# Performance work log

Hardware: AMD Instinct MI355X
Metric: run time of the kernel (lower is better)

The kernel has to match this reference:

```python
import jax, jax.numpy as jnp
import numpy as np

EMBED_DIM = 1024
NUM_HEADS = 16
HEAD_DIM = EMBED_DIM // NUM_HEADS


def setup_inputs() -> dict:
    key = jax.random.key(0)
    k_x, k_wqkv, k_bqkv, k_wo, k_bo = jax.random.split(key, 5)
    B, T, C = 4, 2048, EMBED_DIM
    s_in = 1.0 / np.sqrt(C)
    return {
        "x": jax.random.normal(k_x, (B, T, C), dtype=jnp.float32),
        # torch Linear: weight [out,in]; we store transposed [in,out] for x @ W
        "w_qkv": jax.random.uniform(k_wqkv, (C, 3 * C), dtype=jnp.float32, minval=-s_in, maxval=s_in),
        "b_qkv": jax.random.uniform(k_bqkv, (3 * C,), dtype=jnp.float32, minval=-s_in, maxval=s_in),
        "w_out": jax.random.uniform(k_wo, (C, C), dtype=jnp.float32, minval=-s_in, maxval=s_in),
        "b_out": jax.random.uniform(k_bo, (C,), dtype=jnp.float32, minval=-s_in, maxval=s_in),
    }


def reference(x, w_qkv, b_qkv, w_out, b_out):
    B, T, C = x.shape
    H, D = NUM_HEADS, HEAD_DIM
    qkv = x @ w_qkv + b_qkv                       # [B,T,3C]
    qkv = qkv.reshape(B, T, 3, H, D)
    q, k, v = qkv[:, :, 0], qkv[:, :, 1], qkv[:, :, 2]   # [B,T,H,D]
    q = q.transpose(0, 2, 1, 3)                   # [B,H,T,D]
    k = k.transpose(0, 2, 1, 3)
    v = v.transpose(0, 2, 1, 3)
    scale = 1.0 / np.sqrt(D).astype(np.float32)
    att = jnp.einsum("bhqd,bhkd->bhqk", q, k) * scale   # [B,H,T,T]
    causal = jnp.tril(jnp.ones((T, T), dtype=bool))
    att = jnp.where(causal[None, None], att, -jnp.inf)
    att = jax.nn.softmax(att, axis=-1)
    y = jnp.einsum("bhqk,bhkd->bhqd", att, v)     # [B,H,T,D]
    y = y.transpose(0, 2, 1, 3).reshape(B, T, C)
    return y @ w_out + b_out
```

## Files before the change

kernel.cpp:

```cpp
#include <hip/hip_runtime.h>
#include <hip/hip_bf16.h>

#define EMBED 1024
#define NHEAD 16
#define HDIM  64
#define BATCH 4
#define SEQ   2048
#define BT    (BATCH*SEQ)
#define NQKV  (3*EMBED)

using bf16x8 = __attribute__((ext_vector_type(8))) short;
using f32x4  = __attribute__((ext_vector_type(4))) float;

__device__ __forceinline__ unsigned short f2bf(float f){
  union { float f; unsigned u; } v; v.f = f;
  unsigned r = v.u + 0x7FFFu + ((v.u >> 16) & 1u);
  return (unsigned short)(r >> 16);
}

__device__ __forceinline__ float exp2_hw(float x){
  float r; asm("v_exp_f32 %0, %1" : "=v"(r) : "v"(x)); return r;
}
__device__ __forceinline__ unsigned cvtpk_bf16(float lo, float hi){
  unsigned r; asm("v_cvt_pk_bf16_f32 %0, %1, %2" : "=v"(r) : "v"(lo), "v"(hi));
  return r;
}

__device__ __forceinline__ void gload_lds16(const void* g, void* l){
  __builtin_amdgcn_global_load_lds(
      (const __attribute__((address_space(1))) void*)g,
      (__attribute__((address_space(3))) void*)l, 16, 0, 0);
}

__global__ __launch_bounds__(256) void cvt_f32_bf16_k(
    const float* __restrict__ in, unsigned short* __restrict__ out, int n)
{
  int i = (blockIdx.x * 256 + threadIdx.x) * 4;
  if (i >= n) return;
  float4 v = *(const float4*)&in[i];
  ushort4 o;
  o.x = f2bf(v.x); o.y = f2bf(v.y); o.z = f2bf(v.z); o.w = f2bf(v.w);
  *(ushort4*)&out[i] = o;
}

__global__ __launch_bounds__(256) void transpose_cvt_k(
    const float* __restrict__ in, unsigned short* __restrict__ out, int R, int C)
{
  __shared__ float tile[32][33];
  int tx = threadIdx.x, ty = threadIdx.y;
  int c0 = blockIdx.x * 32, r0 = blockIdx.y * 32;
#pragma unroll
  for (int j = ty; j < 32; j += 8)
    tile[j][tx] = in[(size_t)(r0 + j) * C + c0 + tx];
  __syncthreads();
#pragma unroll
  for (int j = ty; j < 32; j += 8)
    out[(size_t)(c0 + j) * R + r0 + tx] = f2bf(tile[tx][j]);
}

template<int EPI>
__global__ __launch_bounds__(256) void gemm_bt(
    const unsigned short* __restrict__ A,
    const unsigned short* __restrict__ Bt,
    const float* __restrict__ bias,
    unsigned short* __restrict__ qp,
    unsigned short* __restrict__ kp,
    unsigned short* __restrict__ vp,
    float* __restrict__ outp,
    int M, int N, int K)
{
  __shared__ unsigned short As[2][128 * 64];
  __shared__ unsigned short Bs[2][128 * 64];
  const int tid = threadIdx.x;
  const int w = tid >> 6, lane = tid & 63;
  const int lr = lane & 15, lg = lane >> 4;
  const int gy = gridDim.y;
  const int lin = (int)(blockIdx.y * gridDim.x + blockIdx.x);
  const int cpx = (int)(gridDim.x * gy) >> 3;
  const int wg = (lin & 7) * cpx + (lin >> 3);
  const int m0 = (wg / gy) * 128, n0 = (wg % gy) * 128;
  const int wm = (w >> 1) * 64, wn = (w & 1) * 64;
  const int fbase = w * 4;
  f32x4 acc[4][4] = {};

  int srow[4], scol[4];
#pragma unroll
  for (int i = 0; i < 4; i++) {
    int f = (fbase + i) * 64 + lane;
    srow[i] = f >> 3;
    scol[i] = (f & 7) * 8;
  }

  const int nkt = K >> 6;

#pragma unroll
  for (int i = 0; i < 4; i++) {
    gload_lds16(A  + (size_t)(m0 + srow[i]) * K + scol[i], &As[0][(fbase + i) * 512]);
    gload_lds16(Bt + (size_t)(n0 + srow[i]) * K + scol[i], &Bs[0][(fbase + i) * 512]);
  }

  int cur = 0;
  for (int t = 0; t < nkt; t++) {
    if (t + 1 < nkt) {
      const int kt = (t + 1) << 6;
#pragma unroll
      for (int i = 0; i < 4; i++) {
        gload_lds16(A  + (size_t)(m0 + srow[i]) * K + kt + scol[i],
                    &As[cur ^ 1][(fbase + i) * 512]);
        gload_lds16(Bt + (size_t)(n0 + srow[i]) * K + kt + scol[i],
                    &Bs[cur ^ 1][(fbase + i) * 512]);
      }
      asm volatile("s_waitcnt vmcnt(8)" ::: "memory");
    } else {
      asm volatile("s_waitcnt vmcnt(0)" ::: "memory");
    }
    __builtin_amdgcn_s_barrier();
    __builtin_amdgcn_sched_barrier(0);

#pragma unroll
    for (int kk = 0; kk < 2; kk++) {
      bf16x8 af[4], bv[4];
#pragma unroll
      for (int mi = 0; mi < 4; mi++)
        af[mi] = *(const bf16x8*)&As[cur][(wm + mi * 16 + lr) * 64 + kk * 32 + lg * 8];
#pragma unroll
      for (int ni = 0; ni < 4; ni++)
        bv[ni] = *(const bf16x8*)&Bs[cur][(wn + ni * 16 + lr) * 64 + kk * 32 + lg * 8];
      __builtin_amdgcn_s_setprio(1);
#pragma unroll
      for (int mi = 0; mi < 4; mi++)
#pragma unroll
        for (int ni = 0; ni < 4; ni++)
          acc[mi][ni] = __builtin_amdgcn_mfma_f32_16x16x32_bf16(af[mi], bv[ni], acc[mi][ni], 0, 0, 0);
      __builtin_amdgcn_s_setprio(0);
    }

    asm volatile("s_waitcnt lgkmcnt(0)" ::: "memory");
    __builtin_amdgcn_s_barrier();
    cur ^= 1;
  }

#pragma unroll
  for (int mi = 0; mi < 4; mi++)
#pragma unroll
    for (int ni = 0; ni < 4; ni++) {
      const int rowb = m0 + wm + mi * 16 + lg * 4;
      const int colb = n0 + wn + ni * 16 + lr;
      const float bv_ = bias[colb];
      if (EPI == 0) {
        int s = colb >> 10, hh = (colb & 1023) >> 6, d = colb & 63;
        int b = rowb >> 11, t = rowb & 2047;
        if (s == 2) {
          ushort4 o4;
          o4.x = f2bf(acc[mi][ni][0] + bv_);
          o4.y = f2bf(acc[mi][ni][1] + bv_);
          o4.z = f2bf(acc[mi][ni][2] + bv_);
          o4.w = f2bf(acc[mi][ni][3] + bv_);
          *(ushort4*)&vp[((size_t)(b * NHEAD + hh) * HDIM + d) * SEQ + t] = o4;
        } else {
          unsigned short* dst = (s == 0) ? qp : kp;
          const float scl = (s == 0) ? 0.18033688f : 1.0f;
#pragma unroll
          for (int r = 0; r < 4; r++)
            dst[((size_t)(b * NHEAD + hh) * SEQ + t + r) * HDIM + d] =
                f2bf((acc[mi][ni][r] + bv_) * scl);
        }
      } else {
#pragma unroll
        for (int r = 0; r < 4; r++)
          outp[(size_t)(rowb + r) * N + colb] = acc[mi][ni][r] + bv_;
      }
    }
}

__device__ __forceinline__ void softmax_frag(
    f32x4 (&s)[4], float& m, f32x4& su, f32x4 (&o)[4],
    unsigned short* psrow, int qrow, int kbase, bool needmask,
    int lg, int lr, int pswz)
{
  const float NEG = -1e30f;
  if (needmask) {
#pragma unroll
    for (int n = 0; n < 4; n++)
#pragma unroll
      for (int r = 0; r < 4; r++) {
        if (kbase + n * 16 + lg * 4 + r > qrow) s[n][r] = NEG;
      }
  }
  float t0 = fmaxf(fmaxf(s[0][0], s[0][1]), fmaxf(s[0][2], s[0][3]));
  float t1 = fmaxf(fmaxf(s[1][0], s[1][1]), fmaxf(s[1][2], s[1][3]));
  float t2 = fmaxf(fmaxf(s[2][0], s[2][1]), fmaxf(s[2][2], s[2][3]));
  float t3 = fmaxf(fmaxf(s[3][0], s[3][1]), fmaxf(s[3][2], s[3][3]));
  float pm = fmaxf(fmaxf(t0, t1), fmaxf(t2, t3));
  if (__any(pm > m + 8.f)) {
    pm = fmaxf(pm, __shfl_xor(pm, 16, 64));
    pm = fmaxf(pm, __shfl_xor(pm, 32, 64));
    float mn = fmaxf(m, pm);
    float fac = exp2_hw(m - mn);
    m = mn;
    float fr[4];
#pragma unroll
    for (int r = 0; r < 4; r++) fr[r] = __shfl(fac, lg * 4 + r, 64);
#pragma unroll
    for (int r = 0; r < 4; r++) su[r] *= fr[r];
#pragma unroll
    for (int n = 0; n < 4; n++)
#pragma unroll
      for (int r = 0; r < 4; r++) o[n][r] *= fr[r];
  }
#pragma unroll
  for (int n = 0; n < 4; n++) {
    float p0 = exp2_hw(s[n][0] - m);
    float p1 = exp2_hw(s[n][1] - m);
    float p2 = exp2_hw(s[n][2] - m);
    float p3 = exp2_hw(s[n][3] - m);
    uint2 pk;
    pk.x = cvtpk_bf16(p0, p1);
    pk.y = cvtpk_bf16(p2, p3);
    int E = (lr * 64 + n * 16 + lg * 4) ^ pswz;
    *(uint2*)&psrow[E] = pk;
  }
}

__global__ __launch_bounds__(256) void attn_k(
    const unsigned short* __restrict__ Q,
    const unsigned short* __restrict__ K,
    const unsigned short* __restrict__ Vt,
    unsigned short* __restrict__ Y)
{
  __shared__ unsigned short Ks[2][64 * 64];
  __shared__ unsigned short Vs[2][64 * 64];
  __shared__ unsigned short Ps[4][32 * 64];

  const int tid = threadIdx.x;
  const int w = tid >> 6, lane = tid & 63;
  const int lr = lane & 15, lg = lane >> 4;
  const int bh = blockIdx.y;
  const int b = bh >> 4, h = bh & 15;
  const size_t base = (size_t)bh * SEQ * HDIM;
  const float NEG = -1e30f;
  const int pswz = (lr & 7) << 3;

  bf16x8 ones;
#pragma unroll
  for (int e = 0; e < 8; e++) ones[e] = (short)0x3F80;

  const int f0 = w * 128 + lane, f1 = f0 + 64;
  const int r0_ = f0 >> 3, c0_ = ((f0 & 7) ^ (r0_ & 7)) * 8;
  const int r1_ = f1 >> 3, c1_ = ((f1 & 7) ^ (r1_ & 7)) * 8;

  for (int seg = 0; seg < 2; seg++) {
    const int qb = seg ? (int)blockIdx.x : (15 - (int)blockIdx.x);
    const int qw0 = qb * 128 + w * 32;
    const int nk = 2 * qb + 2;

    bf16x8 aq[2][2];
#pragma unroll
    for (int f = 0; f < 2; f++)
#pragma unroll
      for (int kk = 0; kk < 2; kk++)
        aq[f][kk] = *(const bf16x8*)
            &Q[base + (size_t)(qw0 + f * 16 + lr) * HDIM + kk * 32 + lg * 8];

    f32x4 o0[4] = {}, o1[4] = {};
    f32x4 su0 = {}, su1 = {};
    float m0 = NEG, m1 = NEG;

    {
      const unsigned short* kxp = K + base;
      const unsigned short* vxp = Vt + base;
      gload_lds16(kxp + r0_ * HDIM + c0_, &Ks[0][f0 * 8]);
      gload_lds16(kxp + r1_ * HDIM + c1_, &Ks[0][f1 * 8]);
      gload_lds16(vxp + (size_t)r0_ * SEQ + c0_, &Vs[0][f0 * 8]);
      gload_lds16(vxp + (size_t)r1_ * SEQ + c1_, &Vs[0][f1 * 8]);
    }
    __syncthreads();

    int cur = 0;
    for (int kb = 0; kb < nk; kb++) {
      if (kb + 1 < nk) {
        const unsigned short* kxp = K + base + (size_t)(kb + 1) * 64 * HDIM;
        const unsigned short* vxp = Vt + base + (kb + 1) * 64;
        gload_lds16(kxp + r0_ * HDIM + c0_, &Ks[cur ^ 1][f0 * 8]);
        gload_lds16(kxp + r1_ * HDIM + c1_, &Ks[cur ^ 1][f1 * 8]);
        gload_lds16(vxp + (size_t)r0_ * SEQ + c0_, &Vs[cur ^ 1][f0 * 8]);
        gload_lds16(vxp + (size_t)r1_ * SEQ + c1_, &Vs[cur ^ 1][f1 * 8]);
      }

      const bool active = (kb * 64 <= qw0 + 31);
      if (active) {
        f32x4 s0[4] = {}, s1[4] = {};
        __builtin_amdgcn_s_setprio(1);
#pragma unroll
        for (int kk = 0; kk < 2; kk++) {
          bf16x8 bk[4];
#pragma unroll
          for (int n = 0; n < 4; n++) {
            int E = (n * 16 + lr) * 64 + kk * 32 + lg * 8;
            bk[n] = *(const bf16x8*)&Ks[cur][E ^ pswz];
          }
#pragma unroll
          for (int n = 0; n < 4; n++) {
            s0[n] = __builtin_amdgcn_mfma_f32_16x16x32_bf16(bk[n], aq[0][kk], s0[n], 0, 0, 0);
            s1[n] = __builtin_amdgcn_mfma_f32_16x16x32_bf16(bk[n], aq[1][kk], s1[n], 0, 0, 0);
          }
        }
        __builtin_amdgcn_s_setprio(0);

        const int kbase = kb * 64;
        softmax_frag(s0, m0, su0, o0, &Ps[w][0],
                     qw0 + lr, kbase, kbase + 63 > qw0, lg, lr, pswz);
        softmax_frag(s1, m1, su1, o1, &Ps[w][16 * 64],
                     qw0 + 16 + lr, kbase, kbase + 63 > qw0 + 16, lg, lr, pswz);

        __builtin_amdgcn_s_setprio(1);
#pragma unroll
        for (int kc = 0; kc < 2; kc++) {
          bf16x8 ap0 = *(const bf16x8*)&Ps[w][(lr * 64 + kc * 32 + lg * 8) ^ pswz];
          bf16x8 ap1 = *(const bf16x8*)&Ps[w][((16 + lr) * 64 + kc * 32 + lg * 8) ^ pswz];
          su0 = __builtin_amdgcn_mfma_f32_16x16x32_bf16(ap0, ones, su0, 0, 0, 0);
          su1 = __builtin_amdgcn_mfma_f32_16x16x32_bf16(ap1, ones, su1, 0, 0, 0);
#pragma unroll
          for (int n = 0; n < 4; n++) {
            int E = (n * 16 + lr) * 64 + kc * 32 + lg * 8;
            bf16x8 bv = *(const bf16x8*)&Vs[cur][E ^ pswz];
            o0[n] = __builtin_amdgcn_mfma_f32_16x16x32_bf16(ap0, bv, o0[n], 0, 0, 0);
            o1[n] = __builtin_amdgcn_mfma_f32_16x16x32_bf16(ap1, bv, o1[n], 0, 0, 0);
          }
        }
        __builtin_amdgcn_s_setprio(0);
      }

      __syncthreads();
      cur ^= 1;
    }

    float inv0[4], inv1[4];
#pragma unroll
    for (int r = 0; r < 4; r++) { inv0[r] = 1.f / su0[r]; inv1[r] = 1.f / su1[r]; }
#pragma unroll
    for (int n = 0; n < 4; n++)
#pragma unroll
      for (int r = 0; r < 4; r++) {
        int col = h * HDIM + n * 16 + lr;
        int t0 = qw0 + lg * 4 + r;
        Y[((size_t)(b * SEQ + t0)) * EMBED + col] = f2bf(o0[n][r] * inv0[r]);
        int t1 = qw0 + 16 + lg * 4 + r;
        Y[((size_t)(b * SEQ + t1)) * EMBED + col] = f2bf(o1[n][r] * inv1[r]);
      }
  }
}

extern "C" void kernel_launch(void* const* d_in, const int* in_sizes, int n_in,
                              void* d_out, int out_size, void* d_ws, size_t ws_size,
                              hipStream_t stream) {
  const float* x     = (const float*)d_in[0];
  const float* w_qkv = (const float*)d_in[1];
  const float* b_qkv = (const float*)d_in[2];
  const float* w_out = (const float*)d_in[3];
  const float* b_out = (const float*)d_in[4];
  float* outp = (float*)d_out;

  char* ws = (char*)d_ws;
  unsigned short* xb    = (unsigned short*)ws; ws += (size_t)BT * EMBED * 2;
  unsigned short* wqkvT = (unsigned short*)ws; ws += (size_t)NQKV * EMBED * 2;
  unsigned short* woutT = (unsigned short*)ws; ws += (size_t)EMBED * EMBED * 2;
  unsigned short* Qb    = (unsigned short*)ws; ws += (size_t)BATCH * NHEAD * SEQ * HDIM * 2;
  unsigned short* Kb    = (unsigned short*)ws; ws += (size_t)BATCH * NHEAD * SEQ * HDIM * 2;
  unsigned short* Vb    = (unsigned short*)ws; ws += (size_t)BATCH * NHEAD * SEQ * HDIM * 2;
  unsigned short* Yb    = (unsigned short*)ws; ws += (size_t)BT * EMBED * 2;

  cvt_f32_bf16_k<<<(BT * EMBED) / 1024, 256, 0, stream>>>(x, xb, BT * EMBED);
  transpose_cvt_k<<<dim3(NQKV / 32, EMBED / 32), dim3(32, 8), 0, stream>>>(w_qkv, wqkvT, EMBED, NQKV);
  transpose_cvt_k<<<dim3(EMBED / 32, EMBED / 32), dim3(32, 8), 0, stream>>>(w_out, woutT, EMBED, EMBED);

  gemm_bt<0><<<dim3(BT / 128, NQKV / 128), 256, 0, stream>>>(
      xb, wqkvT, b_qkv, Qb, Kb, Vb, nullptr, BT, NQKV, EMBED);

  attn_k<<<dim3(8, BATCH * NHEAD), 256, 0, stream>>>(Qb, Kb, Vb, Yb);

  gemm_bt<1><<<dim3(BT / 128, EMBED / 128), 256, 0, stream>>>(
      Yb, woutT, b_out, nullptr, nullptr, nullptr, outp, BT, EMBED, EMBED);
}
```

Measured before the change: 201.7 us.

## Use 128x192 tiles with 6 waves for the QKV projection GEMM

Splits the templated GEMM into a dedicated QKV kernel with a 128x192 output tile, 384 threads (6 waves in a 2x3 grid) and a unified double-buffered LDS region loaded via direct global-to-LDS copies. The larger N tile raises A-tile reuse and cuts the grid from 1536 to 1024 blocks, aiming to reduce global traffic per FLOP in the largest GEMM. LDS per block rises to about 80 KB and the load distribution across waves is uneven (40 chunks over 6 waves), which may affect occupancy and wait-count correctness.

```diff
diff --git a/kernel.cpp b/kernel.cpp
--- a/kernel.cpp
+++ b/kernel.cpp
@@ -58,14 +58,120 @@
     out[(size_t)(c0 + j) * R + r0 + tx] = f2bf(tile[tx][j]);
 }
 
-template<int EPI>
-__global__ __launch_bounds__(256) void gemm_bt(
+__global__ __launch_bounds__(384) void gemm_qkv(
     const unsigned short* __restrict__ A,
     const unsigned short* __restrict__ Bt,
     const float* __restrict__ bias,
     unsigned short* __restrict__ qp,
     unsigned short* __restrict__ kp,
     unsigned short* __restrict__ vp,
+    int M, int N, int K)
+{
+  __shared__ unsigned short Ls[2][(128 + 192) * 64];
+  const int tid = threadIdx.x;
+  const int w = tid >> 6, lane = tid & 63;
+  const int lr = lane & 15, lg = lane >> 4;
+  const int wr = w / 3, wc = w % 3;
+  const int wm = wr * 64, wn = wc * 64;
+
+  const int gy = gridDim.y;
+  const int lin = (int)(blockIdx.y * gridDim.x + blockIdx.x);
+  const int cpx = (int)(gridDim.x * gy) >> 3;
+  const int wg = (lin & 7) * cpx + (lin >> 3);
+  const int m0 = (wg / gy) * 128, n0 = (wg % gy) * 192;
+
+  f32x4 acc[4][4] = {};
+
+  const unsigned short* gp[7];
+  int ldst[7];
+#pragma unroll
+  for (int i = 0; i < 7; i++) {
+    int c = w + 6 * i;
+    if (c < 40) {
+      ldst[i] = c * 512;
+      if (c < 16) { int f = c * 64 + lane;        gp[i] = A  + (size_t)(m0 + (f >> 3)) * K + (f & 7) * 8; }
+      else        { int f = (c - 16) * 64 + lane; gp[i] = Bt + (size_t)(n0 + (f >> 3)) * K + (f & 7) * 8; }
+    } else { gp[i] = A; ldst[i] = 0; }
+  }
+
+  const int nkt = K >> 6;
+
+#pragma unroll
+  for (int i = 0; i < 7; i++) {
+    int c = w + 6 * i;
+    if (c < 40) gload_lds16(gp[i], &Ls[0][ldst[i]]);
+  }
+
+  int cur = 0;
+  for (int t = 0; t < nkt; t++) {
+    if (t + 1 < nkt) {
+      const int kt = (t + 1) << 6;
+#pragma unroll
+      for (int i = 0; i < 7; i++) {
+        int c = w + 6 * i;
+        if (c < 40) gload_lds16(gp[i] + kt, &Ls[cur ^ 1][ldst[i]]);
+      }
+      asm volatile("s_waitcnt vmcnt(6)" ::: "memory");
+    } else {
+      asm volatile("s_waitcnt vmcnt(0)" ::: "memory");
+    }
+    __builtin_amdgcn_s_barrier();
+    __builtin_amdgcn_sched_barrier(0);
+
+#pragma unroll
+    for (int kk = 0; kk < 2; kk++) {
+      bf16x8 af[4], bv[4];
+#pragma unroll
+      for (int mi = 0; mi < 4; mi++)
+        af[mi] = *(const bf16x8*)&Ls[cur][(wm + mi * 16 + lr) * 64 + kk * 32 + lg * 8];
+#pragma unroll
+      for (int ni = 0; ni < 4; ni++)
+        bv[ni] = *(const bf16x8*)&Ls[cur][8192 + (wn + ni * 16 + lr) * 64 + kk * 32 + lg * 8];
+      __builtin_amdgcn_s_setprio(1);
+#pragma unroll
+      for (int mi = 0; mi < 4; mi++)
+#pragma unroll
+        for (int ni = 0; ni < 4; ni++)
+          acc[mi][ni] = __builtin_amdgcn_mfma_f32_16x16x32_bf16(af[mi], bv[ni], acc[mi][ni], 0, 0, 0);
+      __builtin_amdgcn_s_setprio(0);
+    }
+
+    asm volatile("s_waitcnt lgkmcnt(0)" ::: "memory");
+    __builtin_amdgcn_s_barrier();
+    cur ^= 1;
+  }
+
+#pragma unroll
+  for (int mi = 0; mi < 4; mi++)
+#pragma unroll
+    for (int ni = 0; ni < 4; ni++) {
+      const int rowb = m0 + wm + mi * 16 + lg * 4;
+      const int colb = n0 + wn + ni * 16 + lr;
+      const float bv_ = bias[colb];
+      int s = colb >> 10, hh = (colb & 1023) >> 6, d = colb & 63;
+      int b = rowb >> 11, t = rowb & 2047;
+      if (s == 2) {
+        ushort4 o4;
+        o4.x = f2bf(acc[mi][ni][0] + bv_);
+        o4.y = f2bf(acc[mi][ni][1] + bv_);
+        o4.z = f2bf(acc[mi][ni][2] + bv_);
+        o4.w = f2bf(acc[mi][ni][3] + bv_);
+        *(ushort4*)&vp[((size_t)(b * NHEAD + hh) * HDIM + d) * SEQ + t] = o4;
+      } else {
+        unsigned short* dst = (s == 0) ? qp : kp;
+        const float scl = (s == 0) ? 0.18033688f : 1.0f;
+#pragma unroll
+        for (int r = 0; r < 4; r++)
+          dst[((size_t)(b * NHEAD + hh) * SEQ + t + r) * HDIM + d] =
+              f2bf((acc[mi][ni][r] + bv_) * scl);
+      }
+    }
+}
+
+__global__ __launch_bounds__(256) void gemm_out(
+    const unsigned short* __restrict__ A,
+    const unsigned short* __restrict__ Bt,
+    const float* __restrict__ bias,
     float* __restrict__ outp,
     int M, int N, int K)
 {
@@ -147,29 +253,9 @@
       const int rowb = m0 + wm + mi * 16 + lg * 4;
       const int colb = n0 + wn + ni * 16 + lr;
       const float bv_ = bias[colb];
-      if (EPI == 0) {
-        int s = colb >> 10, hh = (colb & 1023) >> 6, d = colb & 63;
-        int b = rowb >> 11, t = rowb & 2047;
-        if (s == 2) {
-          ushort4 o4;
-          o4.x = f2bf(acc[mi][ni][0] + bv_);
-          o4.y = f2bf(acc[mi][ni][1] + bv_);
-          o4.z = f2bf(acc[mi][ni][2] + bv_);
-          o4.w = f2bf(acc[mi][ni][3] + bv_);
-          *(ushort4*)&vp[((size_t)(b * NHEAD + hh) * HDIM + d) * SEQ + t] = o4;
-        } else {
-          unsigned short* dst = (s == 0) ? qp : kp;
-          const float scl = (s == 0) ? 0.18033688f : 1.0f;
-#pragma unroll
-          for (int r = 0; r < 4; r++)
-            dst[((size_t)(b * NHEAD + hh) * SEQ + t + r) * HDIM + d] =
-                f2bf((acc[mi][ni][r] + bv_) * scl);
-        }
-      } else {
-#pragma unroll
-        for (int r = 0; r < 4; r++)
-          outp[(size_t)(rowb + r) * N + colb] = acc[mi][ni][r] + bv_;
-      }
+#pragma unroll
+      for (int r = 0; r < 4; r++)
+        outp[(size_t)(rowb + r) * N + colb] = acc[mi][ni][r] + bv_;
     }
 }
 
@@ -374,11 +460,11 @@
   transpose_cvt_k<<<dim3(NQKV / 32, EMBED / 32), dim3(32, 8), 0, stream>>>(w_qkv, wqkvT, EMBED, NQKV);
   transpose_cvt_k<<<dim3(EMBED / 32, EMBED / 32), dim3(32, 8), 0, stream>>>(w_out, woutT, EMBED, EMBED);
 
-  gemm_bt<0><<<dim3(BT / 128, NQKV / 128), 256, 0, stream>>>(
-      xb, wqkvT, b_qkv, Qb, Kb, Vb, nullptr, BT, NQKV, EMBED);
+  gemm_qkv<<<dim3(BT / 128, NQKV / 192), 384, 0, stream>>>(
+      xb, wqkvT, b_qkv, Qb, Kb, Vb, BT, NQKV, EMBED);
 
   attn_k<<<dim3(8, BATCH * NHEAD), 256, 0, stream>>>(Qb, Kb, Vb, Yb);
 
-  gemm_bt<1><<<dim3(BT / 128, EMBED / 128), 256, 0, stream>>>(
-      Yb, woutT, b_out, nullptr, nullptr, nullptr, outp, BT, EMBED, EMBED);
-}
+  gemm_out<<<dim3(BT / 128, EMBED / 128), 256, 0, stream>>>(
+      Yb, woutT, b_out, outp, BT, EMBED, EMBED);
+}
```

Result: slower. 217.3 us (+7.7%).
